# Kernel optimization log

Measured on AMD Instinct MI355X. Metric: run time of the kernel, lower is better.

The kernel has to match this reference:

```python
import jax, jax.numpy as jnp
import numpy as np

TEMPERATURE = 0.07
BASE_TEMPERATURE = 0.07
EPS = 1e-10


def setup_inputs() -> dict:
    key = jax.random.key(0)
    k1, k2, k3 = jax.random.split(key, 3)
    bsz, n_views, d = 4096, 2, 256
    features = jax.random.normal(k1, (bsz, n_views, d), dtype=jnp.float32)
    # L2-normalize views as is standard for SupCon inputs (keeps logits sane)
    features = features / jnp.linalg.norm(features, axis=-1, keepdims=True)
    va_labels = jax.random.normal(k2, (bsz, 2), dtype=jnp.float32)
    batch_belong_diaID = jax.random.randint(k3, (bsz,), 0, 512, dtype=jnp.int64)
    return {
        "features": features,
        "va_labels": va_labels,
        "batch_belong_diaID": batch_belong_diaID,
        "thres_dict": 1,
    }


def reference(features, va_labels, batch_belong_diaID, thres_dict):
    bsz, n_views, d = features.shape
    dtype = features.dtype

    # --- vectorized mask construction (replaces O(bsz^2) python loops) ---
    eye = jnp.eye(bsz, dtype=bool)
    same_dia = batch_belong_diaID[:, None] == batch_belong_diaID[None, :]
    diff = va_labels[:, None, :] - va_labels[None, :, :]          # [bsz, bsz, 2]
    euclid = jnp.sqrt(jnp.sum(diff * diff, axis=-1))              # [bsz, bsz]
    close_va = euclid < thres_dict
    # final mask: diagonal | same dialogue | VA-close (off-diag terms; diag already 1)
    mask = (eye | same_dia | close_va).astype(dtype)
    mask = jax.lax.stop_gradient(mask)  # mask build is non-differentiable in torch too

    # --- contrastive loss (contrast_mode='one') ---
    # torch.cat(torch.unbind(features, 1), 0): view-major stacking
    contrast_feature = features.transpose(1, 0, 2).reshape(n_views * bsz, d)
    anchor_feature = features[:, 0]                               # anchor_count = 1

    logits = jnp.matmul(anchor_feature, contrast_feature.T) / TEMPERATURE  # [bsz, n_views*bsz]
    logits = logits - jax.lax.stop_gradient(jnp.max(logits, axis=1, keepdims=True))

    mask_t = jnp.tile(mask, (1, n_views))                          # [bsz, n_views*bsz]
    # logits_mask: zero out self-contrast (column i for anchor row i)
    idx = jnp.arange(bsz)
    logits_mask = jnp.ones((bsz, n_views * bsz), dtype=dtype).at[idx, idx].set(0.0)
    mask_t = mask_t * logits_mask

    exp_logits = jnp.exp(logits) * logits_mask
    log_prob = logits - jnp.log(jnp.sum(exp_logits, axis=1, keepdims=True) + EPS)

    mean_log_prob_pos = jnp.sum(mask_t * log_prob, axis=1) / (jnp.sum(mask_t, axis=1) + EPS)
    loss = jnp.mean(-mean_log_prob_pos)  # anchor_count=1 -> plain mean over bsz
    return loss
```

## Files before the change

### kernel.cpp

```cpp
#include <hip/hip_runtime.h>
#include <hip/hip_bf16.h>

#define BSZ   4096
#define NCON  8192
#define DFEAT 256
#define INV_T 14.285714285714285f

#define BJ 32
#define BI 128
#define NJT 8
#define JSTRIP (NJT * BJ)

typedef __attribute__((ext_vector_type(8))) short short8;
typedef __attribute__((ext_vector_type(4))) float f32x4;

__device__ __forceinline__ unsigned short f2bf(float f) {
    __hip_bfloat16 h = __float2bfloat16(f);
    return *reinterpret_cast<unsigned short*>(&h);
}

__device__ __forceinline__ void gload_lds16(const void* g, void* l) {
    __builtin_amdgcn_global_load_lds(
        (const __attribute__((address_space(1))) unsigned int*)g,
        (__attribute__((address_space(3))) unsigned int*)l,
        16, 0, 0);
}

__device__ __forceinline__ void gload_reg16(const void* p, short8& dst) {
    unsigned long long a = (unsigned long long)p;
    asm volatile("global_load_dwordx4 %0, %1, off"
                 : "=v"(dst) : "v"(a));
}


__global__ __launch_bounds__(256) void k_prep(const float* __restrict__ feat,
                                              unsigned short* __restrict__ con,
                                              float* __restrict__ acc) {
    int idx = blockIdx.x * 256 + threadIdx.x;
    int e = idx * 4;
    int j = e >> 8;
    int k = e & 255;
    int src = (j < BSZ) ? ((j * 2) * DFEAT + k)
                        : (((j - BSZ) * 2 + 1) * DFEAT + k);
    float4 f = *(const float4*)(feat + src);
    ushort4 o;
    o.x = f2bf(f.x); o.y = f2bf(f.y); o.z = f2bf(f.z); o.w = f2bf(f.w);
    *(ushort4*)(con + e) = o;
    if (idx < 3 * BSZ) acc[idx] = 0.0f;
}

__global__ __launch_bounds__(256, 2) void k_main(const __hip_bfloat16* __restrict__ conp,
                                                 const float* __restrict__ va,
                                                 const int* __restrict__ dia,
                                                 const int* __restrict__ thr_ptr,
                                                 float* __restrict__ Srow,
                                                 float* __restrict__ Arow,
                                                 float* __restrict__ Brow) {
    __shared__ short lX[2][BJ * DFEAT];
    __shared__ float s_vjx[JSTRIP], s_vjy[JSTRIP];
    __shared__ int   s_dj[JSTRIP];

    const int tid  = threadIdx.x;
    const int lane = tid & 63;
    const int wv   = tid >> 6;
    const int l15  = lane & 15;
    const int hi   = lane >> 4;
    const int jstrip0 = blockIdx.x * JSTRIP;
    const int ibase   = blockIdx.y * BI + wv * 32;
    const short* cs = (const short*)conp;

    auto stageX = [&](int buf, int jt) {
        #pragma unroll
        for (int q = 0; q < 4; ++q) {
            int e   = q * 2048 + tid * 8;
            int col = e & 63;
            int row = (e >> 6) & 31;
            int k2  = e >> 11;
            int scol = col ^ ((row & 7) << 3);
            gload_lds16(cs + (size_t)(jstrip0 + jt * BJ + row) * DFEAT + k2 * 64 + scol,
                        &lX[buf][e]);
        }
    };

    stageX(0, 0);

    const short* yrow0 = cs + (size_t)(ibase + l15) * DFEAT + hi * 8;
    short8 y[2][8];
    #pragma unroll
    for (int n = 0; n < 2; ++n)
        #pragma unroll
        for (int s = 0; s < 8; ++s)
            gload_reg16(yrow0 + (size_t)n * 16 * DFEAT + s * 32, y[n][s]);

    if (tid < JSTRIP) {
        int jm = (jstrip0 + tid) & (BSZ - 1);
        s_vjx[tid] = va[2 * jm]; s_vjy[tid] = va[2 * jm + 1]; s_dj[tid] = dia[jm];
    }

    int raw = *thr_ptr;
    float t_ = (raw > 0 && raw < 100000) ? (float)raw : __int_as_float(raw);
    float thres2 = t_ * t_;

    float vix[2], viy[2]; int di[2];
    #pragma unroll
    for (int n = 0; n < 2; ++n) {
        int i = ibase + n * 16 + l15;
        vix[n] = va[2 * i]; viy[n] = va[2 * i + 1]; di[n] = dia[i];
    }

    float sp[2] = {0.f, 0.f};
    float ap[2] = {0.f, 0.f};
    float bp[2] = {0.f, 0.f};

    __syncthreads();
    asm volatile("s_waitcnt vmcnt(0)" ::: "memory");
    __builtin_amdgcn_sched_barrier(0);

    for (int jt = 0; jt < NJT; ++jt) {
        const int cur = jt & 1;
        if (jt < NJT - 1) stageX(cur ^ 1, jt + 1);

        f32x4 acc[2][2];
        #pragma unroll
        for (int m = 0; m < 2; ++m)
            #pragma unroll
            for (int n = 0; n < 2; ++n)
                acc[m][n] = (f32x4){0.f, 0.f, 0.f, 0.f};

        const char* bufX = (const char*)&lX[cur][0];
        #pragma unroll
        for (int s = 0; s < 8; ++s) {
            const int base = (s >> 1) * 4096;
            const int colb = (s & 1) * 64 + hi * 16;
            short8 xf[2];
            #pragma unroll
            for (int m = 0; m < 2; ++m) {
                int row = m * 16 + l15;
                xf[m] = *(const short8*)(bufX + base + row * 128 + (colb ^ ((row & 7) << 4)));
            }
            #pragma unroll
            for (int m = 0; m < 2; ++m)
                #pragma unroll
                for (int n = 0; n < 2; ++n)
                    acc[m][n] = __builtin_amdgcn_mfma_f32_16x16x32_bf16(xf[m], y[n][s], acc[m][n], 0, 0, 0);
        }

        const int jt0 = jt * BJ;
        #pragma unroll
        for (int m = 0; m < 2; ++m) {
            #pragma unroll
            for (int r = 0; r < 4; ++r) {
                const int jl = m * 16 + hi * 4 + r;
                const int j  = jstrip0 + jt0 + jl;
                const int jm = j & (BSZ - 1);
                float vjx = s_vjx[jt0 + jl], vjy = s_vjy[jt0 + jl];
                int dj = s_dj[jt0 + jl];
                #pragma unroll
                for (int n = 0; n < 2; ++n) {
                    const int i = ibase + n * 16 + l15;
                    float l = __builtin_fmaf(acc[m][n][r], INV_T, -INV_T);
                    bool lm = (j != i);
                    float e = lm ? __expf(l) : 0.0f;
                    float dx = vix[n] - vjx, dy = viy[n] - vjy;
                    bool mk = (i == jm) | (di[n] == dj) | (dx * dx + dy * dy < thres2);
                    sp[n] += e;
                    if (mk & lm) { ap[n] += l; bp[n] += 1.0f; }
                }
            }
        }
        __syncthreads();
    }

    #pragma unroll
    for (int n = 0; n < 2; ++n) {
        float s = sp[n], a = ap[n], b = bp[n];
        s += __shfl_xor(s, 16, 64);  a += __shfl_xor(a, 16, 64);  b += __shfl_xor(b, 16, 64);
        s += __shfl_xor(s, 32, 64);  a += __shfl_xor(a, 32, 64);  b += __shfl_xor(b, 32, 64);
        if (hi == 0) {
            int i = ibase + n * 16 + l15;
            atomicAdd(&Srow[i], s);
            atomicAdd(&Arow[i], a);
            atomicAdd(&Brow[i], b);
        }
    }
}

__global__ __launch_bounds__(256) void k_final(const float* __restrict__ S,
                                               const float* __restrict__ A,
                                               const float* __restrict__ B,
                                               float* __restrict__ out) {
    __shared__ float red[256];
    float sum = 0.f;
    for (int i = threadIdx.x; i < BSZ; i += 256) {
        float b = B[i];
        float v = (A[i] - b * logf(S[i] + 1e-10f)) / (b + 1e-10f);
        sum += -v;
    }
    red[threadIdx.x] = sum;
    __syncthreads();
    for (int s = 128; s > 0; s >>= 1) {
        if (threadIdx.x < s) red[threadIdx.x] += red[threadIdx.x + s];
        __syncthreads();
    }
    if (threadIdx.x == 0) out[0] = red[0] / (float)BSZ;
}

extern "C" void kernel_launch(void* const* d_in, const int* in_sizes, int n_in,
                              void* d_out, int out_size, void* d_ws, size_t ws_size,
                              hipStream_t stream) {
    const float* feat = (const float*)d_in[0];
    const float* va   = (const float*)d_in[1];
    const int*   dia  = (const int*)d_in[2];
    const int*   thr  = (const int*)d_in[3];

    unsigned short* con = (unsigned short*)d_ws;
    float* acc = (float*)((char*)d_ws + (size_t)NCON * DFEAT * 2);
    float* out = (float*)d_out;

    k_prep<<<(NCON * DFEAT / 4 + 255) / 256, 256, 0, stream>>>(feat, con, acc);

    dim3 grid(NCON / JSTRIP, BSZ / BI);
    k_main<<<grid, 256, 0, stream>>>((const __hip_bfloat16*)con, va, dia, thr,
                                     acc, acc + BSZ, acc + 2 * BSZ);

    k_final<<<1, 256, 0, stream>>>(acc, acc + BSZ, acc + 2 * BSZ, out);
}
```

Baseline: 51.02 us.

## Process both contrast views per column tile to share mask computation

Each block now stages the view-0 and view-1 contrast rows for the same sample index together, so the grid covers only BSZ columns instead of NCON. The mask terms (VA distance, dialogue id, diagonal) are computed once per column and applied to both views' logits, and the masked sums use branchless FMAs instead of a conditional. This halves the mask arithmetic and the shared-memory metadata loads, but doubles LDS use per block (about 64KB for the X buffers) and the accumulator registers. That may lower occupancy and halves the number of blocks.

```diff
diff --git a/kernel.cpp b/kernel.cpp
--- a/kernel.cpp
+++ b/kernel.cpp
@@ -6,10 +6,10 @@
 #define DFEAT 256
 #define INV_T 14.285714285714285f
 
-#define BJ 32
+#define BJM 32
 #define BI 128
 #define NJT 8
-#define JSTRIP (NJT * BJ)
+#define JSTRIP_M (NJT * BJM)
 
 typedef __attribute__((ext_vector_type(8))) short short8;
 typedef __attribute__((ext_vector_type(4))) float f32x4;
@@ -56,29 +56,33 @@
                                                  float* __restrict__ Srow,
                                                  float* __restrict__ Arow,
                                                  float* __restrict__ Brow) {
-    __shared__ short lX[2][BJ * DFEAT];
-    __shared__ float s_vjx[JSTRIP], s_vjy[JSTRIP];
-    __shared__ int   s_dj[JSTRIP];
+    __shared__ short lX[2][2][BJM * DFEAT];
+    __shared__ float s_vjx[JSTRIP_M], s_vjy[JSTRIP_M];
+    __shared__ int   s_dj[JSTRIP_M];
 
     const int tid  = threadIdx.x;
     const int lane = tid & 63;
     const int wv   = tid >> 6;
     const int l15  = lane & 15;
     const int hi   = lane >> 4;
-    const int jstrip0 = blockIdx.x * JSTRIP;
-    const int ibase   = blockIdx.y * BI + wv * 32;
+    const int jmbase = blockIdx.x * JSTRIP_M;
+    const int ibase  = blockIdx.y * BI + wv * 32;
     const short* cs = (const short*)conp;
 
     auto stageX = [&](int buf, int jt) {
         #pragma unroll
-        for (int q = 0; q < 4; ++q) {
-            int e   = q * 2048 + tid * 8;
-            int col = e & 63;
-            int row = (e >> 6) & 31;
-            int k2  = e >> 11;
-            int scol = col ^ ((row & 7) << 3);
-            gload_lds16(cs + (size_t)(jstrip0 + jt * BJ + row) * DFEAT + k2 * 64 + scol,
-                        &lX[buf][e]);
+        for (int v = 0; v < 2; ++v) {
+            #pragma unroll
+            for (int q = 0; q < 4; ++q) {
+                int e   = q * 2048 + tid * 8;
+                int col = e & 63;
+                int row = (e >> 6) & 31;
+                int k2  = e >> 11;
+                int scol = col ^ ((row & 7) << 3);
+                gload_lds16(cs + (size_t)(jmbase + jt * BJM + row + v * BSZ) * DFEAT
+                               + k2 * 64 + scol,
+                            &lX[buf][v][e]);
+            }
         }
     };
 
@@ -92,8 +96,8 @@
         for (int s = 0; s < 8; ++s)
             gload_reg16(yrow0 + (size_t)n * 16 * DFEAT + s * 32, y[n][s]);
 
-    if (tid < JSTRIP) {
-        int jm = (jstrip0 + tid) & (BSZ - 1);
+    if (tid < JSTRIP_M) {
+        int jm = jmbase + tid;
         s_vjx[tid] = va[2 * jm]; s_vjy[tid] = va[2 * jm + 1]; s_dj[tid] = dia[jm];
     }
 
@@ -120,51 +124,64 @@
         const int cur = jt & 1;
         if (jt < NJT - 1) stageX(cur ^ 1, jt + 1);
 
-        f32x4 acc[2][2];
-        #pragma unroll
-        for (int m = 0; m < 2; ++m)
-            #pragma unroll
-            for (int n = 0; n < 2; ++n)
-                acc[m][n] = (f32x4){0.f, 0.f, 0.f, 0.f};
-
-        const char* bufX = (const char*)&lX[cur][0];
+        f32x4 acc[2][2][2];
+        #pragma unroll
+        for (int v = 0; v < 2; ++v)
+            #pragma unroll
+            for (int m = 0; m < 2; ++m)
+                #pragma unroll
+                for (int n = 0; n < 2; ++n)
+                    acc[v][m][n] = (f32x4){0.f, 0.f, 0.f, 0.f};
+
         #pragma unroll
         for (int s = 0; s < 8; ++s) {
             const int base = (s >> 1) * 4096;
             const int colb = (s & 1) * 64 + hi * 16;
-            short8 xf[2];
-            #pragma unroll
-            for (int m = 0; m < 2; ++m) {
-                int row = m * 16 + l15;
-                xf[m] = *(const short8*)(bufX + base + row * 128 + (colb ^ ((row & 7) << 4)));
-            }
-            #pragma unroll
-            for (int m = 0; m < 2; ++m)
-                #pragma unroll
-                for (int n = 0; n < 2; ++n)
-                    acc[m][n] = __builtin_amdgcn_mfma_f32_16x16x32_bf16(xf[m], y[n][s], acc[m][n], 0, 0, 0);
-        }
-
-        const int jt0 = jt * BJ;
+            short8 xf[2][2];
+            #pragma unroll
+            for (int v = 0; v < 2; ++v)
+                #pragma unroll
+                for (int m = 0; m < 2; ++m) {
+                    int row = m * 16 + l15;
+                    xf[v][m] = *(const short8*)((const char*)&lX[cur][v][0]
+                                 + base + row * 128 + (colb ^ ((row & 7) << 4)));
+                }
+            #pragma unroll
+            for (int v = 0; v < 2; ++v)
+                #pragma unroll
+                for (int m = 0; m < 2; ++m)
+                    #pragma unroll
+                    for (int n = 0; n < 2; ++n)
+                        acc[v][m][n] = __builtin_amdgcn_mfma_f32_16x16x32_bf16(
+                            xf[v][m], y[n][s], acc[v][m][n], 0, 0, 0);
+        }
+
+        const int jt0 = jt * BJM;
         #pragma unroll
         for (int m = 0; m < 2; ++m) {
             #pragma unroll
             for (int r = 0; r < 4; ++r) {
-                const int jl = m * 16 + hi * 4 + r;
-                const int j  = jstrip0 + jt0 + jl;
-                const int jm = j & (BSZ - 1);
-                float vjx = s_vjx[jt0 + jl], vjy = s_vjy[jt0 + jl];
-                int dj = s_dj[jt0 + jl];
+                const int jl  = jt0 + m * 16 + hi * 4 + r;
+                const int jmg = jmbase + jl;
+                float vjx = s_vjx[jl], vjy = s_vjy[jl];
+                int dj = s_dj[jl];
                 #pragma unroll
                 for (int n = 0; n < 2; ++n) {
                     const int i = ibase + n * 16 + l15;
-                    float l = __builtin_fmaf(acc[m][n][r], INV_T, -INV_T);
-                    bool lm = (j != i);
-                    float e = lm ? __expf(l) : 0.0f;
+                    float a0 = acc[0][m][n][r], a1 = acc[1][m][n][r];
+                    float l0 = __builtin_fmaf(a0, INV_T, -INV_T);
+                    float l1 = __builtin_fmaf(a1, INV_T, -INV_T);
                     float dx = vix[n] - vjx, dy = viy[n] - vjy;
-                    bool mk = (i == jm) | (di[n] == dj) | (dx * dx + dy * dy < thres2);
-                    sp[n] += e;
-                    if (mk & lm) { ap[n] += l; bp[n] += 1.0f; }
+                    bool diag = (i == jmg);
+                    bool mk = diag | (di[n] == dj) | (dx * dx + dy * dy < thres2);
+                    float e0 = diag ? 0.0f : __expf(l0);
+                    float e1 = __expf(l1);
+                    sp[n] += e0 + e1;
+                    float msel  = mk ? 1.0f : 0.0f;
+                    float msel0 = (mk & !diag) ? 1.0f : 0.0f;
+                    ap[n] = __builtin_fmaf(msel0, l0, ap[n]);
+                    ap[n] = __builtin_fmaf(msel,  l1, ap[n]);
+                    bp[n] += msel0 + msel;
                 }
             }
         }
@@ -219,7 +236,7 @@
 
     k_prep<<<(NCON * DFEAT / 4 + 255) / 256, 256, 0, stream>>>(feat, con, acc);
 
-    dim3 grid(NCON / JSTRIP, BSZ / BI);
+    dim3 grid(BSZ / JSTRIP_M, BSZ / BI);
     k_main<<<grid, 256, 0, stream>>>((const __hip_bfloat16*)con, va, dia, thr,
                                      acc, acc + BSZ, acc + 2 * BSZ);
 
```

Result: faster. 43.55 us (-14.6%).
